# Performance work log

Measured on AMD Instinct MI355X. Metric: run time of the kernel, lower is better.

## Reference

```python
import jax, jax.numpy as jnp
import numpy as np

N = 2048          # num agents / graph nodes
D = 128           # n_actor == n_map
ALPHA = 0.2       # GAT leakyrelu alpha
NEG = -1e9
X_IDX = [4, 9, 14, 19]   # actors_inter_cat time indices per LSTM step
E_IDX = [0, 4, 9, 14]    # graph_adjs time indices per LSTM step


def setup_inputs() -> dict:
    key = jax.random.key(0)
    ks = jax.random.split(key, 10)
    xavier = lambda k, shape: jax.random.uniform(
        k, shape, jnp.float32, -1.0, 1.0) * 1.414 * np.sqrt(6.0 / (shape[-2] + shape[-1]))
    actors_inter_cat = jax.random.normal(ks[0], (N, 20, D), jnp.float32)
    graph_adjs = jax.random.randint(ks[1], (N, 20, N), 0, 2, jnp.int32)
    # 4 GAT_SRF gates (forget, input, input_cell, output), stacked on leading axis
    Wg = xavier(ks[2], (4, 2 * D, D))          # gate projection W: in=2*D, out=D
    ag = xavier(ks[3], (4, 2 * D))             # attention vector a (2*out_features,)
    W = xavier(ks[4], (D, D))                  # GAT cell output projection
    b = xavier(ks[5], (1, D))
    h0 = xavier(ks[6], (1, D))
    conv_w = jax.random.normal(ks[7], (3, D, D, 2), jnp.float32) * (1.0 / np.sqrt(2 * D))
    conv_b = jax.random.normal(ks[8], (3, D), jnp.float32) * 0.01
    return {"actors_inter_cat": actors_inter_cat, "graph_adjs": graph_adjs,
            "Wg": Wg, "ag": ag, "W": W, "b": b, "h0": h0,
            "conv_w": conv_w, "conv_b": conv_b}


def _gat_gates(gin, mask, Wg, ag):
    # gin: (N, 2D); mask: (N, N) bool. Computes all 4 GAT_SRF gates at once.
    Wh = jnp.einsum('nf,gfo->gno', gin, Wg)                 # (4, N, D)
    s_src = jnp.einsum('gno,go->gn', Wh, ag[:, :D])         # a^T [Wh_i ..]
    s_dst = jnp.einsum('gno,go->gn', Wh, ag[:, D:])
    e = jax.nn.leaky_relu(s_src[:, :, None] + s_dst[:, None, :], ALPHA)  # (4,N,N)
    e = jnp.where(mask[None], e, NEG)
    attn = jax.nn.softmax(e, axis=-1)
    return jax.nn.elu(jnp.einsum('gnm,gmo->gno', attn, Wh))  # concat=True -> ELU


def reference(actors_inter_cat, graph_adjs, Wg, ag, W, b, h0, conv_w, conv_b):
    n = actors_inter_cat.shape[0]
    cell = actors_inter_cat[:, 0, :]
    hidden = jnp.broadcast_to(h0, (n, D))
    outs = []
    for t in range(4):  # fixed 4-step recurrence
        X = actors_inter_cat[:, X_IDX[t], :]
        mask = graph_adjs[:, E_IDX[t], :] > 0
        gin = jnp.concatenate([X, hidden], axis=1)          # (N, 2D)
        g = _gat_gates(gin, mask, Wg, ag)                   # (4, N, D)
        forget = jax.nn.sigmoid(g[0])
        inp_gate = jax.nn.sigmoid(g[1])
        inp_cell = jnp.tanh(g[2])
        out_gate = jax.nn.sigmoid(g[3])
        cell = cell * forget + inp_gate * inp_cell
        hidden = jnp.tanh(cell) * out_gate
        outs.append(jax.nn.sigmoid(hidden @ W + b))
    y = jnp.stack(outs, axis=2)                             # (N, D, 4)
    for l in range(3):  # kernel-2 Conv1d stack: length 4 -> 3 -> 2 -> 1
        y = (jnp.einsum('nct,oc->not', y[:, :, :-1], conv_w[l, :, :, 0])
             + jnp.einsum('nct,oc->not', y[:, :, 1:], conv_w[l, :, :, 1])
             + conv_b[l][None, :, None])
    return y[:, :, 0]                                       # squeeze -> (N, D)
```

## Files before the change

### kernel.cpp

```cpp
#include <hip/hip_runtime.h>

typedef __attribute__((ext_vector_type(8))) short short8;
typedef __attribute__((ext_vector_type(4))) float floatx4;

#define MFMA16(a,b,c) __builtin_amdgcn_mfma_f32_16x16x32_bf16(a,b,c,0,0,0)

__device__ __forceinline__ unsigned short f2bf(float f){
  unsigned u = __float_as_uint(f);
  u += 0x7fffu + ((u >> 16) & 1u);
  return (unsigned short)(u >> 16);
}
__device__ __forceinline__ float sigm(float x){ return 1.f/(1.f+__expf(-x)); }


__global__ __launch_bounds__(256) void prep_kernel(const float* __restrict__ actors,
    const float* __restrict__ Wg, const float* __restrict__ cw, const int* __restrict__ adj,
    float* __restrict__ cell, unsigned short* __restrict__ WgA, float* __restrict__ cwT,
    unsigned long long* __restrict__ bm){
  int bid = blockIdx.x;
  if (bid < 1024){
    int idx = bid*256 + threadIdx.x;
    int n = idx >> 7, c = idx & 127;
    cell[idx] = actors[(size_t)n*2560 + c];
  } else if (bid < 1536){
    int e = (bid-1024)*256 + threadIdx.x;
    int g = e >> 15, o = (e >> 8) & 127, k = e & 255;
    unsigned short v = f2bf(Wg[(size_t)g*32768 + k*128 + o]);
    int off = ((o>>4)*8 + (k>>5))*512 + (((k>>3)&3)*16 + (o&15))*8 + (k&7);
    WgA[(size_t)g*32768 + off] = v;
  } else if (bid < 1728){
    int e = (bid-1536)*256 + threadIdx.x;
    int l = e >> 14, rr = e & 16383, k = rr >> 7, o = rr & 127;
    cwT[(size_t)l*32768 + k*256 + o]       = cw[(size_t)l*32768 + o*256 + k*2];
    cwT[(size_t)l*32768 + k*256 + 128 + o] = cw[(size_t)l*32768 + o*256 + k*2 + 1];
  } else {
    const int E[4] = {0,4,9,14};
    int mb = bid - 1728;
    int t = mb & 3, nblk = mb >> 2;
    int wv = threadIdx.x >> 6, lane = threadIdx.x & 63;
    int n = nblk*4 + wv;
    const int* row = adj + (size_t)n*40960 + (size_t)E[t]*2048;
    unsigned long long* outp = bm + ((size_t)t*2048 + n)*32;
    for (int it=0; it<32; ++it){
      unsigned long long bal = __ballot(row[it*64 + lane] > 0);
      if (lane == 0) outp[it] = bal;
    }
  }
}

__global__ __launch_bounds__(256) void gatewh_kernel(const float* __restrict__ actors,
    const float* __restrict__ gbuf, float* __restrict__ cell, const float* __restrict__ h0,
    const float* __restrict__ W, const float* __restrict__ bvec,
    const unsigned short* __restrict__ WgA, const float* __restrict__ ag,
    float* __restrict__ y, unsigned short* __restrict__ WhB,
    float* __restrict__ s_src, float* __restrict__ s_dst, int xoff, int t){
  __shared__ float hl[16][132];
  __shared__ __align__(16) unsigned short ginb[16*264];
  __shared__ float sredS[4][4][16], sredD[4][4][16];
  int n0 = blockIdx.x*16, tid = threadIdx.x;
  int row = tid>>4, o0 = (tid&15)*8;
  if (t == 0){
    const float* hp = h0 + o0;
    #pragma unroll
    for (int j=0;j<8;++j) hl[row][o0+j] = hp[j];
  } else {
    size_t idx = (size_t)(n0+row)*128 + o0;
    float4 ga0 = *(const float4*)(gbuf+idx),          ga1 = *(const float4*)(gbuf+idx+4);
    float4 gb0 = *(const float4*)(gbuf+262144+idx),   gb1 = *(const float4*)(gbuf+262144+idx+4);
    float4 gc0 = *(const float4*)(gbuf+524288+idx),   gc1 = *(const float4*)(gbuf+524288+idx+4);
    float4 gd0 = *(const float4*)(gbuf+786432+idx),   gd1 = *(const float4*)(gbuf+786432+idx+4);
    float4 c0 = *(const float4*)(cell+idx),           c1 = *(const float4*)(cell+idx+4);
    float fgv[8] = {ga0.x,ga0.y,ga0.z,ga0.w,ga1.x,ga1.y,ga1.z,ga1.w};
    float igv[8] = {gb0.x,gb0.y,gb0.z,gb0.w,gb1.x,gb1.y,gb1.z,gb1.w};
    float icv[8] = {gc0.x,gc0.y,gc0.z,gc0.w,gc1.x,gc1.y,gc1.z,gc1.w};
    float ogv[8] = {gd0.x,gd0.y,gd0.z,gd0.w,gd1.x,gd1.y,gd1.z,gd1.w};
    float cv[8]  = {c0.x,c0.y,c0.z,c0.w,c1.x,c1.y,c1.z,c1.w};
    float cl[8], hd[8];
    #pragma unroll
    for (int j=0;j<8;++j){
      cl[j] = cv[j]*sigm(fgv[j]) + sigm(igv[j])*tanhf(icv[j]);
      hd[j] = tanhf(cl[j])*sigm(ogv[j]);
      hl[row][o0+j] = hd[j];
    }
    *(float4*)(cell+idx)   = (float4){cl[0],cl[1],cl[2],cl[3]};
    *(float4*)(cell+idx+4) = (float4){cl[4],cl[5],cl[6],cl[7]};
  }
  __syncthreads();
  if (t >= 1){
    float acc[8];
    float4 b0 = *(const float4*)(bvec+o0), b1 = *(const float4*)(bvec+o0+4);
    acc[0]=b0.x;acc[1]=b0.y;acc[2]=b0.z;acc[3]=b0.w;acc[4]=b1.x;acc[5]=b1.y;acc[6]=b1.z;acc[7]=b1.w;
    for (int k=0;k<128;++k){
      float hv = hl[row][k];
      float4 w0 = *(const float4*)(W + (size_t)k*128 + o0);
      float4 w1 = *(const float4*)(W + (size_t)k*128 + o0 + 4);
      acc[0]+=hv*w0.x; acc[1]+=hv*w0.y; acc[2]+=hv*w0.z; acc[3]+=hv*w0.w;
      acc[4]+=hv*w1.x; acc[5]+=hv*w1.y; acc[6]+=hv*w1.z; acc[7]+=hv*w1.w;
    }
    float* yp = y + (size_t)(t-1)*262144 + (size_t)(n0+row)*128 + o0;
    #pragma unroll
    for (int j=0;j<8;++j) yp[j] = sigm(acc[j]);
  }
  {
    const float* ap = actors + (size_t)(n0+row)*2560 + xoff + o0;
    float4 a = *(const float4*)ap, bb = *(const float4*)(ap+4);
    unsigned short tmp[8] = {f2bf(a.x),f2bf(a.y),f2bf(a.z),f2bf(a.w),
                             f2bf(bb.x),f2bf(bb.y),f2bf(bb.z),f2bf(bb.w)};
    *(uint4*)&ginb[row*264 + o0] = *(const uint4*)tmp;
    unsigned short tmp2[8];
    #pragma unroll
    for (int j=0;j<8;++j) tmp2[j] = f2bf(hl[row][o0+j]);
    *(uint4*)&ginb[row*264 + 128 + o0] = *(const uint4*)tmp2;
  }
  __syncthreads();
  int w = tid>>6, lane = tid&63, quad = lane>>4, l16 = lane&15;
  int m32 = blockIdx.x>>1, min32 = (blockIdx.x&1)*16 + l16;
  int qp = min32>>3, jp = min32&7;
  for (int g=0; g<4; ++g){
    floatx4 acc0 = {0.f,0.f,0.f,0.f}, acc1 = acc0;
    const unsigned short* wa = WgA + (size_t)g*32768;
    #pragma unroll
    for (int kh=0; kh<8; ++kh){
      short8 bfr = *(const short8*)&ginb[l16*264 + kh*32 + quad*8];
      short8 a0 = *(const short8*)(wa + (size_t)(((w*2+0)*8 + kh)*64 + lane)*8);
      short8 a1 = *(const short8*)(wa + (size_t)(((w*2+1)*8 + kh)*64 + lane)*8);
      acc0 = MFMA16(a0, bfr, acc0);
      acc1 = MFMA16(a1, bfr, acc1);
    }
    float ps = 0.f, pd = 0.f;
    unsigned short* wb = WhB + (size_t)(g*8 + w*2)*32768 + m32*512 + qp*128 + jp;
    const float* agp = ag + g*256;
    #pragma unroll
    for (int i=0;i<2;++i){
      floatx4 ac = i ? acc1 : acc0;
      #pragma unroll
      for (int r=0;r<4;++r){
        int o = w*32 + i*16 + quad*4 + r;
        float v = ac[r];
        ps += v*agp[o]; pd += v*agp[128+o];
        wb[i*32768 + (quad*4+r)*8] = f2bf(v);
      }
    }
    ps += __shfl_down(ps,32); ps += __shfl_down(ps,16);
    pd += __shfl_down(pd,32); pd += __shfl_down(pd,16);
    if (lane < 16){ sredS[g][w][l16] = ps; sredD[g][w][l16] = pd; }
  }
  __syncthreads();
  if (tid < 128){
    int g = tid>>5, which = (tid>>4)&1, n = tid&15;
    float s;
    if (which) s = sredD[g][0][n]+sredD[g][1][n]+sredD[g][2][n]+sredD[g][3][n];
    else       s = sredS[g][0][n]+sredS[g][1][n]+sredS[g][2][n]+sredS[g][3][n];
    (which ? s_dst : s_src)[g*2048 + n0 + n] = s;
  }
}

__global__ __launch_bounds__(512) void attn_kernel(const unsigned char* __restrict__ bmb,
    const unsigned short* __restrict__ WhB, const float* __restrict__ s_src,
    const float* __restrict__ s_dst, float* __restrict__ gout, int t){
  __shared__ float obuf[4][16][132];
  __shared__ float zpart[8][16];
  int g = blockIdx.y, n0 = blockIdx.x*16, tid = threadIdx.x;
  int w = tid>>6, lane = tid&63, quad = lane>>4, l16 = lane&15;
  float srcv = s_src[g*2048 + n0 + l16];
  const float* sd = s_dst + g*2048;
  const unsigned char* mrow = bmb + ((size_t)t*2048 + n0 + l16)*256 + w*32;
  uint4 q0 = *(const uint4*)mrow, q1 = *(const uint4*)(mrow+16);
  unsigned mwd[8] = {q0.x,q0.y,q0.z,q0.w, q1.x,q1.y,q1.z,q1.w};
  const unsigned short* wb = WhB + (size_t)g*262144;
  float z0 = 0.f;
  floatx4 acc[8];
  #pragma unroll
  for (int j=0;j<8;++j) acc[j] = (floatx4){0.f,0.f,0.f,0.f};
  #pragma unroll
  for (int c=0; c<8; ++c){
    int mk = w*256 + c*32 + quad*8;
    float4 sa = *(const float4*)(sd + mk);
    float4 sb = *(const float4*)(sd + mk + 4);
    unsigned mb = (mwd[c] >> (quad*8)) & 0xffu;
    float sv[8] = {sa.x,sa.y,sa.z,sa.w,sb.x,sb.y,sb.z,sb.w};
    short8 A0;
    #pragma unroll
    for (int j=0;j<8;++j){
      float s = srcv + sv[j];
      s = s > 0.f ? s : 0.2f*s;
      float p = ((mb >> j) & 1u) ? __expf(s) : 0.f;
      z0 += p;
      A0[j] = (short)f2bf(p);
    }
    const unsigned short* bp = wb + (size_t)(w*8 + c)*512 + lane*8;
    #pragma unroll
    for (int o16=0; o16<8; ++o16){
      short8 bfr = *(const short8*)(bp + (size_t)o16*32768);
      acc[o16] = MFMA16(A0, bfr, acc[o16]);
    }
  }
  z0 += __shfl_down(z0,32); z0 += __shfl_down(z0,16);
  if (lane < 16) zpart[w][l16] = z0;
  if (w < 4){
    #pragma unroll
    for (int o16=0;o16<8;++o16)
      #pragma unroll
      for (int r=0;r<4;++r)
        obuf[w][quad*4+r][o16*16+l16] = acc[o16][r];
  }
  __syncthreads();
  if (w >= 4){
    #pragma unroll
    for (int o16=0;o16<8;++o16)
      #pragma unroll
      for (int r=0;r<4;++r)
        obuf[w-4][quad*4+r][o16*16+l16] += acc[o16][r];
  }
  __syncthreads();
  {
    int row = tid>>5, c0 = (tid&31)*4;
    float z = zpart[0][row]+zpart[1][row]+zpart[2][row]+zpart[3][row]
            + zpart[4][row]+zpart[5][row]+zpart[6][row]+zpart[7][row];
    float inv = 1.f / z;
    float* go = gout + (size_t)g*262144 + (size_t)(n0+row)*128 + c0;
    #pragma unroll
    for (int j=0;j<4;++j){
      float v = (obuf[0][row][c0+j] + obuf[1][row][c0+j]
               + obuf[2][row][c0+j] + obuf[3][row][c0+j]) * inv;
      go[j] = v > 0.f ? v : __expf(v) - 1.f;
    }
  }
}

__global__ __launch_bounds__(256) void convgate_kernel(const float* __restrict__ gbuf,
    const float* __restrict__ cell, const float* __restrict__ W, const float* __restrict__ bvec,
    const float* __restrict__ y, const float* __restrict__ cwT, const float* __restrict__ cb,
    float* __restrict__ out){
  __shared__ float hl[4][128];
  __shared__ float ylds[4][128][4];
  int tid = threadIdx.x;
  int r = tid >> 6, oc = (tid & 63)*2;
  int n = blockIdx.x*4 + r;
  size_t idx = (size_t)n*128 + oc;
  {
    float2 g0 = *(const float2*)(gbuf+idx),        g1 = *(const float2*)(gbuf+262144+idx);
    float2 g2 = *(const float2*)(gbuf+524288+idx), g3 = *(const float2*)(gbuf+786432+idx);
    float2 cv = *(const float2*)(cell+idx);
    float fg[2]={g0.x,g0.y}, ig[2]={g1.x,g1.y}, ic[2]={g2.x,g2.y}, og[2]={g3.x,g3.y};
    float cc[2]={cv.x,cv.y};
    #pragma unroll
    for (int j=0;j<2;++j){
      float cl = cc[j]*sigm(fg[j]) + sigm(ig[j])*tanhf(ic[j]);
      hl[r][oc+j] = tanhf(cl)*sigm(og[j]);
    }
  }
  {
    float2 y0 = *(const float2*)(y+idx), y1 = *(const float2*)(y+262144+idx),
           y2 = *(const float2*)(y+524288+idx);
    float a0[2]={y0.x,y0.y}, a1[2]={y1.x,y1.y}, a2[2]={y2.x,y2.y};
    #pragma unroll
    for (int j=0;j<2;++j){
      ylds[r][oc+j][0]=a0[j]; ylds[r][oc+j][1]=a1[j]; ylds[r][oc+j][2]=a2[j];
    }
  }
  __syncthreads();
  {
    float2 bb = *(const float2*)(bvec+oc);
    float acc[2] = {bb.x, bb.y};
    const float* hr = hl[r];
    for (int k=0;k<128;++k){
      float hv = hr[k];
      float2 wv = *(const float2*)(W + (size_t)k*128 + oc);
      acc[0]+=hv*wv.x; acc[1]+=hv*wv.y;
    }
    #pragma unroll
    for (int j=0;j<2;++j) ylds[r][oc+j][3] = sigm(acc[j]);
  }
  __syncthreads();
  {
    float a0[2]={0,0}, a1[2]={0,0}, a2[2]={0,0};
    for (int k=0;k<128;++k){
      float2 w0 = *(const float2*)(cwT + k*256 + oc);
      float2 w1 = *(const float2*)(cwT + k*256 + 128 + oc);
      float4 yv = *(const float4*)&ylds[r][k][0];
      float wa[2]={w0.x,w0.y}, wb2[2]={w1.x,w1.y};
      #pragma unroll
      for (int j=0;j<2;++j){
        a0[j] += yv.x*wa[j] + yv.y*wb2[j];
        a1[j] += yv.y*wa[j] + yv.z*wb2[j];
        a2[j] += yv.z*wa[j] + yv.w*wb2[j];
      }
    }
    float2 bb = *(const float2*)(cb+oc);
    float bbv[2]={bb.x,bb.y};
    __syncthreads();
    #pragma unroll
    for (int j=0;j<2;++j){
      ylds[r][oc+j][0]=a0[j]+bbv[j]; ylds[r][oc+j][1]=a1[j]+bbv[j]; ylds[r][oc+j][2]=a2[j]+bbv[j];
    }
    __syncthreads();
  }
  {
    float a0[2]={0,0}, a1[2]={0,0};
    for (int k=0;k<128;++k){
      float2 w0 = *(const float2*)(cwT + 32768 + k*256 + oc);
      float2 w1 = *(const float2*)(cwT + 32768 + k*256 + 128 + oc);
      float4 yv = *(const float4*)&ylds[r][k][0];
      float wa[2]={w0.x,w0.y}, wb2[2]={w1.x,w1.y};
      #pragma unroll
      for (int j=0;j<2;++j){
        a0[j] += yv.x*wa[j] + yv.y*wb2[j];
        a1[j] += yv.y*wa[j] + yv.z*wb2[j];
      }
    }
    float2 bb = *(const float2*)(cb+128+oc);
    float bbv[2]={bb.x,bb.y};
    __syncthreads();
    #pragma unroll
    for (int j=0;j<2;++j){
      ylds[r][oc+j][0]=a0[j]+bbv[j]; ylds[r][oc+j][1]=a1[j]+bbv[j];
    }
    __syncthreads();
  }
  {
    float a0[2]={0,0};
    for (int k=0;k<128;++k){
      float2 w0 = *(const float2*)(cwT + 65536 + k*256 + oc);
      float2 w1 = *(const float2*)(cwT + 65536 + k*256 + 128 + oc);
      float4 yv = *(const float4*)&ylds[r][k][0];
      a0[0] += yv.x*w0.x + yv.y*w1.x;
      a0[1] += yv.x*w0.y + yv.y*w1.y;
    }
    float2 bb = *(const float2*)(cb+256+oc);
    float2 res = {a0[0]+bb.x, a0[1]+bb.y};
    *(float2*)(out+idx) = res;
  }
}

extern "C" void kernel_launch(void* const* d_in, const int* in_sizes, int n_in,
                              void* d_out, int out_size, void* d_ws, size_t ws_size,
                              hipStream_t stream) {
  const float* actors = (const float*)d_in[0];
  const int*   adj    = (const int*)d_in[1];
  const float* Wg     = (const float*)d_in[2];
  const float* ag     = (const float*)d_in[3];
  const float* W      = (const float*)d_in[4];
  const float* b      = (const float*)d_in[5];
  const float* h0     = (const float*)d_in[6];
  const float* cw     = (const float*)d_in[7];
  const float* cb     = (const float*)d_in[8];
  float* out = (float*)d_out;

  char* ws = (char*)d_ws;
  unsigned long long* bm = (unsigned long long*)ws;
  float* cell          = (float*)(ws + (size_t)(2u<<20));
  unsigned short* WgA  = (unsigned short*)(ws + (size_t)(3u<<20));
  float* cwT           = (float*)(ws + (size_t)3407872);
  float* s_src         = (float*)(ws + (size_t)3932160);
  float* s_dst         = (float*)(ws + (size_t)3932160 + 32768);
  unsigned short* WhB  = (unsigned short*)(ws + (size_t)(4u<<20));
  float* gbuf          = (float*)(ws + (size_t)(7u<<20));
  float* yplanes       = (float*)(ws + (size_t)(11u<<20));

  const int XI[4] = {4, 9, 14, 19};

  prep_kernel<<<3776, 256, 0, stream>>>(actors, Wg, cw, adj, cell, WgA, cwT, bm);
  for (int t=0; t<4; ++t){
    gatewh_kernel<<<128, 256, 0, stream>>>(actors, gbuf, cell, h0, W, b, WgA, ag,
                                           yplanes, WhB, s_src, s_dst, XI[t]*128, t);
    attn_kernel<<<dim3(128,4), 512, 0, stream>>>((const unsigned char*)bm, WhB,
                                                 s_src, s_dst, gbuf, t);
  }
  convgate_kernel<<<512, 256, 0, stream>>>(gbuf, cell, W, b, yplanes, cwT, cb, out);
}
```

Baseline: 600.1 us.

## Split gatewh work across output halves and double attention rows per block

```diff
diff --git a/kernel.cpp b/kernel.cpp
--- a/kernel.cpp
+++ b/kernel.cpp
@@ -48,102 +48,99 @@
   }
 }
 
-__global__ __launch_bounds__(256) void gatewh_kernel(const float* __restrict__ actors,
+__global__ __launch_bounds__(512) void gatewh_kernel(const float* __restrict__ actors,
     const float* __restrict__ gbuf, float* __restrict__ cell, const float* __restrict__ h0,
     const float* __restrict__ W, const float* __restrict__ bvec,
     const unsigned short* __restrict__ WgA, const float* __restrict__ ag,
     float* __restrict__ y, unsigned short* __restrict__ WhB,
-    float* __restrict__ s_src, float* __restrict__ s_dst, int xoff, int t){
+    float* __restrict__ spart, int xoff, int t){
   __shared__ float hl[16][132];
   __shared__ __align__(16) unsigned short ginb[16*264];
   __shared__ float sredS[4][4][16], sredD[4][4][16];
-  int n0 = blockIdx.x*16, tid = threadIdx.x;
-  int row = tid>>4, o0 = (tid&15)*8;
-  if (t == 0){
-    const float* hp = h0 + o0;
-    #pragma unroll
-    for (int j=0;j<8;++j) hl[row][o0+j] = hp[j];
-  } else {
-    size_t idx = (size_t)(n0+row)*128 + o0;
-    float4 ga0 = *(const float4*)(gbuf+idx),          ga1 = *(const float4*)(gbuf+idx+4);
-    float4 gb0 = *(const float4*)(gbuf+262144+idx),   gb1 = *(const float4*)(gbuf+262144+idx+4);
-    float4 gc0 = *(const float4*)(gbuf+524288+idx),   gc1 = *(const float4*)(gbuf+524288+idx+4);
-    float4 gd0 = *(const float4*)(gbuf+786432+idx),   gd1 = *(const float4*)(gbuf+786432+idx+4);
-    float4 c0 = *(const float4*)(cell+idx),           c1 = *(const float4*)(cell+idx+4);
-    float fgv[8] = {ga0.x,ga0.y,ga0.z,ga0.w,ga1.x,ga1.y,ga1.z,ga1.w};
-    float igv[8] = {gb0.x,gb0.y,gb0.z,gb0.w,gb1.x,gb1.y,gb1.z,gb1.w};
-    float icv[8] = {gc0.x,gc0.y,gc0.z,gc0.w,gc1.x,gc1.y,gc1.z,gc1.w};
-    float ogv[8] = {gd0.x,gd0.y,gd0.z,gd0.w,gd1.x,gd1.y,gd1.z,gd1.w};
-    float cv[8]  = {c0.x,c0.y,c0.z,c0.w,c1.x,c1.y,c1.z,c1.w};
-    float cl[8], hd[8];
-    #pragma unroll
-    for (int j=0;j<8;++j){
-      cl[j] = cv[j]*sigm(fgv[j]) + sigm(igv[j])*tanhf(icv[j]);
-      hd[j] = tanhf(cl[j])*sigm(ogv[j]);
-      hl[row][o0+j] = hd[j];
-    }
-    *(float4*)(cell+idx)   = (float4){cl[0],cl[1],cl[2],cl[3]};
-    *(float4*)(cell+idx+4) = (float4){cl[4],cl[5],cl[6],cl[7]};
+  int bx = blockIdx.x;
+  int tile = bx >> 1, ohalf = bx & 1;
+  int n0 = tile*16, tid = threadIdx.x;
+  int row = tid>>5, q = tid&31;
+  {
+    int o0 = q*4;
+    if (t == 0){
+      *(float4*)&hl[row][o0] = *(const float4*)(h0 + o0);
+    } else {
+      size_t idx = (size_t)(n0+row)*128 + o0;
+      float4 ga = *(const float4*)(gbuf+idx);
+      float4 gb = *(const float4*)(gbuf+262144+idx);
+      float4 gc = *(const float4*)(gbuf+524288+idx);
+      float4 gd = *(const float4*)(gbuf+786432+idx);
+      float4 cv = *(const float4*)(cell+idx);
+      float fg[4]={ga.x,ga.y,ga.z,ga.w}, ig[4]={gb.x,gb.y,gb.z,gb.w};
+      float ic[4]={gc.x,gc.y,gc.z,gc.w}, og[4]={gd.x,gd.y,gd.z,gd.w};
+      float cc[4]={cv.x,cv.y,cv.z,cv.w};
+      float clv[4];
+      #pragma unroll
+      for (int j=0;j<4;++j){
+        clv[j] = cc[j]*sigm(fg[j]) + sigm(ig[j])*tanhf(ic[j]);
+        hl[row][o0+j] = tanhf(clv[j])*sigm(og[j]);
+      }
+      if (ohalf == 0)
+        *(float4*)(cell+idx) = (float4){clv[0],clv[1],clv[2],clv[3]};
+    }
   }
   __syncthreads();
   if (t >= 1){
-    float acc[8];
-    float4 b0 = *(const float4*)(bvec+o0), b1 = *(const float4*)(bvec+o0+4);
-    acc[0]=b0.x;acc[1]=b0.y;acc[2]=b0.z;acc[3]=b0.w;acc[4]=b1.x;acc[5]=b1.y;acc[6]=b1.z;acc[7]=b1.w;
-    for (int k=0;k<128;++k){
-      float hv = hl[row][k];
-      float4 w0 = *(const float4*)(W + (size_t)k*128 + o0);
-      float4 w1 = *(const float4*)(W + (size_t)k*128 + o0 + 4);
-      acc[0]+=hv*w0.x; acc[1]+=hv*w0.y; acc[2]+=hv*w0.z; acc[3]+=hv*w0.w;
-      acc[4]+=hv*w1.x; acc[5]+=hv*w1.y; acc[6]+=hv*w1.z; acc[7]+=hv*w1.w;
-    }
-    float* yp = y + (size_t)(t-1)*262144 + (size_t)(n0+row)*128 + o0;
-    #pragma unroll
-    for (int j=0;j<8;++j) yp[j] = sigm(acc[j]);
-  }
-  {
-    const float* ap = actors + (size_t)(n0+row)*2560 + xoff + o0;
+    int oc = ohalf*64 + q*2;
+    float2 bb2 = *(const float2*)(bvec+oc);
+    float a0 = bb2.x, a1 = bb2.y;
+    const float* hr = hl[row];
+    for (int k=0;k<128;++k){
+      float hv = hr[k];
+      float2 wv = *(const float2*)(W + (size_t)k*128 + oc);
+      a0 += hv*wv.x; a1 += hv*wv.y;
+    }
+    float* yp = y + (size_t)(t-1)*262144 + (size_t)(n0+row)*128 + oc;
+    yp[0] = sigm(a0); yp[1] = sigm(a1);
+  }
+  if (q < 16){
+    const float* ap = actors + (size_t)(n0+row)*2560 + xoff + q*8;
     float4 a = *(const float4*)ap, bb = *(const float4*)(ap+4);
     unsigned short tmp[8] = {f2bf(a.x),f2bf(a.y),f2bf(a.z),f2bf(a.w),
                              f2bf(bb.x),f2bf(bb.y),f2bf(bb.z),f2bf(bb.w)};
-    *(uint4*)&ginb[row*264 + o0] = *(const uint4*)tmp;
-    unsigned short tmp2[8];
-    #pragma unroll
-    for (int j=0;j<8;++j) tmp2[j] = f2bf(hl[row][o0+j]);
-    *(uint4*)&ginb[row*264 + 128 + o0] = *(const uint4*)tmp2;
+    *(uint4*)&ginb[row*264 + q*8] = *(const uint4*)tmp;
+  } else {
+    int c0 = (q-16)*8;
+    unsigned short tmp[8];
+    #pragma unroll
+    for (int j=0;j<8;++j) tmp[j] = f2bf(hl[row][c0+j]);
+    *(uint4*)&ginb[row*264 + 128 + c0] = *(const uint4*)tmp;
   }
   __syncthreads();
   int w = tid>>6, lane = tid&63, quad = lane>>4, l16 = lane&15;
-  int m32 = blockIdx.x>>1, min32 = (blockIdx.x&1)*16 + l16;
+  int m32 = tile>>1, min32 = (tile&1)*16 + l16;
   int qp = min32>>3, jp = min32&7;
-  for (int g=0; g<4; ++g){
-    floatx4 acc0 = {0.f,0.f,0.f,0.f}, acc1 = acc0;
+  #pragma unroll
+  for (int ci=0; ci<2; ++ci){
+    int cidx = w*2 + ci;
+    int g = cidx>>2, o16q = cidx&3, o16 = ohalf*4 + o16q;
+    floatx4 acc = {0.f,0.f,0.f,0.f};
     const unsigned short* wa = WgA + (size_t)g*32768;
     #pragma unroll
     for (int kh=0; kh<8; ++kh){
       short8 bfr = *(const short8*)&ginb[l16*264 + kh*32 + quad*8];
-      short8 a0 = *(const short8*)(wa + (size_t)(((w*2+0)*8 + kh)*64 + lane)*8);
-      short8 a1 = *(const short8*)(wa + (size_t)(((w*2+1)*8 + kh)*64 + lane)*8);
-      acc0 = MFMA16(a0, bfr, acc0);
-      acc1 = MFMA16(a1, bfr, acc1);
+      short8 a0 = *(const short8*)(wa + (size_t)((o16*8 + kh)*64 + lane)*8);
+      acc = MFMA16(a0, bfr, acc);
     }
     float ps = 0.f, pd = 0.f;
-    unsigned short* wb = WhB + (size_t)(g*8 + w*2)*32768 + m32*512 + qp*128 + jp;
+    unsigned short* wb = WhB + (size_t)(g*8 + o16)*32768 + m32*512 + qp*128 + jp;
     const float* agp = ag + g*256;
     #pragma unroll
-    for (int i=0;i<2;++i){
-      floatx4 ac = i ? acc1 : acc0;
-      #pragma unroll
-      for (int r=0;r<4;++r){
-        int o = w*32 + i*16 + quad*4 + r;
-        float v = ac[r];
-        ps += v*agp[o]; pd += v*agp[128+o];
-        wb[i*32768 + (quad*4+r)*8] = f2bf(v);
-      }
+    for (int r=0;r<4;++r){
+      int o = o16*16 + quad*4 + r;
+      float v = acc[r];
+      ps += v*agp[o]; pd += v*agp[128+o];
+      wb[(quad*4+r)*8] = f2bf(v);
     }
     ps += __shfl_down(ps,32); ps += __shfl_down(ps,16);
     pd += __shfl_down(pd,32); pd += __shfl_down(pd,16);
-    if (lane < 16){ sredS[g][w][l16] = ps; sredD[g][w][l16] = pd; }
+    if (lane < 16){ sredS[g][o16q][l16] = ps; sredD[g][o16q][l16] = pd; }
   }
   __syncthreads();
   if (tid < 128){
@@ -151,76 +148,96 @@
     float s;
     if (which) s = sredD[g][0][n]+sredD[g][1][n]+sredD[g][2][n]+sredD[g][3][n];
     else       s = sredS[g][0][n]+sredS[g][1][n]+sredS[g][2][n]+sredS[g][3][n];
-    (which ? s_dst : s_src)[g*2048 + n0 + n] = s;
+    spart[(size_t)((ohalf*2 + which)*4 + g)*2048 + n0 + n] = s;
   }
 }
 
 __global__ __launch_bounds__(512) void attn_kernel(const unsigned char* __restrict__ bmb,
-    const unsigned short* __restrict__ WhB, const float* __restrict__ s_src,
-    const float* __restrict__ s_dst, float* __restrict__ gout, int t){
-  __shared__ float obuf[4][16][132];
-  __shared__ float zpart[8][16];
-  int g = blockIdx.y, n0 = blockIdx.x*16, tid = threadIdx.x;
+    const unsigned short* __restrict__ WhB, const float* __restrict__ spart,
+    float* __restrict__ gout, int t){
+  __shared__ float obuf[4][32][132];
+  __shared__ float zpart[8][32];
+  int g = blockIdx.y, n0 = blockIdx.x*32, tid = threadIdx.x;
   int w = tid>>6, lane = tid&63, quad = lane>>4, l16 = lane&15;
-  float srcv = s_src[g*2048 + n0 + l16];
-  const float* sd = s_dst + g*2048;
-  const unsigned char* mrow = bmb + ((size_t)t*2048 + n0 + l16)*256 + w*32;
-  uint4 q0 = *(const uint4*)mrow, q1 = *(const uint4*)(mrow+16);
-  unsigned mwd[8] = {q0.x,q0.y,q0.z,q0.w, q1.x,q1.y,q1.z,q1.w};
+  const float* sS0 = spart + (size_t)(0 + g)*2048;
+  const float* sD0 = spart + (size_t)(4 + g)*2048;
+  const float* sS1 = spart + (size_t)(8 + g)*2048;
+  const float* sD1 = spart + (size_t)(12 + g)*2048;
+  float srcv0 = sS0[n0 + l16]      + sS1[n0 + l16];
+  float srcv1 = sS0[n0 + 16 + l16] + sS1[n0 + 16 + l16];
+  const unsigned char* mr0 = bmb + ((size_t)t*2048 + n0 + l16)*256 + w*32;
+  const unsigned char* mr1 = mr0 + 16*256;
+  uint4 q0 = *(const uint4*)mr0, q1 = *(const uint4*)(mr0+16);
+  uint4 r0 = *(const uint4*)mr1, r1 = *(const uint4*)(mr1+16);
+  unsigned mwd0[8] = {q0.x,q0.y,q0.z,q0.w, q1.x,q1.y,q1.z,q1.w};
+  unsigned mwd1[8] = {r0.x,r0.y,r0.z,r0.w, r1.x,r1.y,r1.z,r1.w};
   const unsigned short* wb = WhB + (size_t)g*262144;
-  float z0 = 0.f;
-  floatx4 acc[8];
+  float z0 = 0.f, z1 = 0.f;
+  floatx4 acc0[8], acc1[8];
   #pragma unroll
-  for (int j=0;j<8;++j) acc[j] = (floatx4){0.f,0.f,0.f,0.f};
+  for (int j=0;j<8;++j){ acc0[j] = (floatx4){0.f,0.f,0.f,0.f}; acc1[j] = acc0[j]; }
   #pragma unroll
   for (int c=0; c<8; ++c){
     int mk = w*256 + c*32 + quad*8;
-    float4 sa = *(const float4*)(sd + mk);
-    float4 sb = *(const float4*)(sd + mk + 4);
-    unsigned mb = (mwd[c] >> (quad*8)) & 0xffu;
-    float sv[8] = {sa.x,sa.y,sa.z,sa.w,sb.x,sb.y,sb.z,sb.w};
-    short8 A0;
+    float4 sa0 = *(const float4*)(sD0 + mk), sb0 = *(const float4*)(sD0 + mk + 4);
+    float4 sa1 = *(const float4*)(sD1 + mk), sb1 = *(const float4*)(sD1 + mk + 4);
+    unsigned mb0 = (mwd0[c] >> (quad*8)) & 0xffu;
+    unsigned mb1 = (mwd1[c] >> (quad*8)) & 0xffu;
+    float sv[8] = {sa0.x+sa1.x, sa0.y+sa1.y, sa0.z+sa1.z, sa0.w+sa1.w,
+                   sb0.x+sb1.x, sb0.y+sb1.y, sb0.z+sb1.z, sb0.w+sb1.w};
+    short8 A0, A1;
     #pragma unroll
     for (int j=0;j<8;++j){
-      float s = srcv + sv[j];
-      s = s > 0.f ? s : 0.2f*s;
-      float p = ((mb >> j) & 1u) ? __expf(s) : 0.f;
-      z0 += p;
-      A0[j] = (short)f2bf(p);
+      float s0 = srcv0 + sv[j];
+      s0 = s0 > 0.f ? s0 : 0.2f*s0;
+      float p0 = ((mb0 >> j) & 1u) ? __expf(s0) : 0.f;
+      z0 += p0;
+      A0[j] = (short)f2bf(p0);
+      float s1 = srcv1 + sv[j];
+      s1 = s1 > 0.f ? s1 : 0.2f*s1;
+      float p1 = ((mb1 >> j) & 1u) ? __expf(s1) : 0.f;
+      z1 += p1;
+      A1[j] = (short)f2bf(p1);
     }
     const unsigned short* bp = wb + (size_t)(w*8 + c)*512 + lane*8;
     #pragma unroll
     for (int o16=0; o16<8; ++o16){
       short8 bfr = *(const short8*)(bp + (size_t)o16*32768);
-      acc[o16] = MFMA16(A0, bfr, acc[o16]);
+      acc0[o16] = MFMA16(A0, bfr, acc0[o16]);
+      acc1[o16] = MFMA16(A1, bfr, acc1[o16]);
     }
   }
   z0 += __shfl_down(z0,32); z0 += __shfl_down(z0,16);
-  if (lane < 16) zpart[w][l16] = z0;
+  z1 += __shfl_down(z1,32); z1 += __shfl_down(z1,16);
+  if (lane < 16){ zpart[w][l16] = z0; zpart[w][16+l16] = z1; }
   if (w < 4){
     #pragma unroll
     for (int o16=0;o16<8;++o16)
       #pragma unroll
-      for (int r=0;r<4;++r)
-        obuf[w][quad*4+r][o16*16+l16] = acc[o16][r];
+      for (int r=0;r<4;++r){
+        obuf[w][quad*4+r][o16*16+l16]      = acc0[o16][r];
+        obuf[w][16+quad*4+r][o16*16+l16]   = acc1[o16][r];
+      }
   }
   __syncthreads();
   if (w >= 4){
     #pragma unroll
     for (int o16=0;o16<8;++o16)
       #pragma unroll
-      for (int r=0;r<4;++r)
-        obuf[w-4][quad*4+r][o16*16+l16] += acc[o16][r];
-  }
-  __syncthreads();
-  {
-    int row = tid>>5, c0 = (tid&31)*4;
+      for (int r=0;r<4;++r){
+        obuf[w-4][quad*4+r][o16*16+l16]    += acc0[o16][r];
+        obuf[w-4][16+quad*4+r][o16*16+l16] += acc1[o16][r];
+      }
+  }
+  __syncthreads();
+  {
+    int row = tid>>4, c0 = (tid&15)*8;
     float z = zpart[0][row]+zpart[1][row]+zpart[2][row]+zpart[3][row]
             + zpart[4][row]+zpart[5][row]+zpart[6][row]+zpart[7][row];
     float inv = 1.f / z;
     float* go = gout + (size_t)g*262144 + (size_t)(n0+row)*128 + c0;
     #pragma unroll
-    for (int j=0;j<4;++j){
+    for (int j=0;j<8;++j){
       float v = (obuf[0][row][c0+j] + obuf[1][row][c0+j]
                + obuf[2][row][c0+j] + obuf[3][row][c0+j]) * inv;
       go[j] = v > 0.f ? v : __expf(v) - 1.f;
@@ -352,8 +369,7 @@
   float* cell          = (float*)(ws + (size_t)(2u<<20));
   unsigned short* WgA  = (unsigned short*)(ws + (size_t)(3u<<20));
   float* cwT           = (float*)(ws + (size_t)3407872);
-  float* s_src         = (float*)(ws + (size_t)3932160);
-  float* s_dst         = (float*)(ws + (size_t)3932160 + 32768);
+  float* spart         = (float*)(ws + (size_t)3932160);
   unsigned short* WhB  = (unsigned short*)(ws + (size_t)(4u<<20));
   float* gbuf          = (float*)(ws + (size_t)(7u<<20));
   float* yplanes       = (float*)(ws + (size_t)(11u<<20));
@@ -362,10 +378,10 @@
 
   prep_kernel<<<3776, 256, 0, stream>>>(actors, Wg, cw, adj, cell, WgA, cwT, bm);
   for (int t=0; t<4; ++t){
-    gatewh_kernel<<<128, 256, 0, stream>>>(actors, gbuf, cell, h0, W, b, WgA, ag,
-                                           yplanes, WhB, s_src, s_dst, XI[t]*128, t);
-    attn_kernel<<<dim3(128,4), 512, 0, stream>>>((const unsigned char*)bm, WhB,
-                                                 s_src, s_dst, gbuf, t);
+    gatewh_kernel<<<256, 512, 0, stream>>>(actors, gbuf, cell, h0, W, b, WgA, ag,
+                                           yplanes, WhB, spart, XI[t]*128, t);
+    attn_kernel<<<dim3(64,4), 512, 0, stream>>>((const unsigned char*)bm, WhB,
+                                                spart, gbuf, t);
   }
   convgate_kernel<<<512, 256, 0, stream>>>(gbuf, cell, W, b, yplanes, cwT, cb, out);
 }
```

Result: no change. 602.9 us, median of 2 (+0.5%).
